# Optimization experiments

Hardware: AMD Instinct MI355X
Metric: run time of the kernel (lower is better)

Reference implementation:

```python
import jax, jax.numpy as jnp
import numpy as np

C = 128
B, H, W = 32, 64, 64


def _lstm(x, Wih, Whh, b, reverse):
    """Batched LSTM, PyTorch gate order (i, f, g, o).
    x: [N, T, C] -> h: [N, T, C]. reverse=True scans backward but returns
    outputs aligned to the original time axis (matches torch bidirectional)."""
    N = x.shape[0]
    Ch = Whh.shape[1]
    xp = jnp.einsum('ntc,gc->ntg', x, Wih) + b  # precomputed input projection [N,T,4C]

    def step(carry, xt):
        h, c = carry
        z = xt + h @ Whh.T
        i, f, g, o = jnp.split(z, 4, axis=-1)
        c = jax.nn.sigmoid(f) * c + jax.nn.sigmoid(i) * jnp.tanh(g)
        h = jax.nn.sigmoid(o) * jnp.tanh(c)
        return (h, c), h

    init = (jnp.zeros((N, Ch), x.dtype), jnp.zeros((N, Ch), x.dtype))
    _, hs = jax.lax.scan(step, init, jnp.swapaxes(xp, 0, 1), reverse=reverse)
    return jnp.swapaxes(hs, 0, 1)


def _conv1x1(x, w, b):
    # x: [B, C, s1, s2]; w: [O, C]; b: [O]
    return jnp.einsum('bcxy,oc->boxy', x, w) + b[None, :, None, None]


def setup_inputs() -> dict:
    key = jax.random.key(0)
    ks = jax.random.split(key, 24)
    k = 1.0 / np.sqrt(C)
    u = lambda kk, shp: jax.random.uniform(kk, shp, jnp.float32, -k, k)
    inp = {'x': jax.random.normal(ks[0], (B, C, H, W), jnp.float32)}
    names = ['vWih_f', 'vWhh_f', 'vb_f', 'vWih_b', 'vWhh_b', 'vb_b',
             'hWih_f', 'hWhh_f', 'hb_f', 'hWih_b', 'hWhh_b', 'hb_b']
    shapes = [(4 * C, C), (4 * C, C), (4 * C,)] * 4
    for i, (n, s) in enumerate(zip(names, shapes)):
        inp[n] = u(ks[1 + i], s)
    for i, n in enumerate(['down', 'up', 'right', 'left']):
        inp['w_' + n] = u(ks[13 + 2 * i], (C, C))
        inp['b_' + n] = u(ks[14 + 2 * i], (C,))
    return inp


def reference(x, vWih_f, vWhh_f, vb_f, vWih_b, vWhh_b, vb_b,
              hWih_f, hWhh_f, hb_f, hWih_b, hWhh_b, hb_b,
              w_down, b_down, w_up, b_up, w_right, b_right, w_left, b_left):
    Bn, Cn, Hn, Wn = x.shape
    xt = jnp.transpose(x, (0, 3, 2, 1))  # [B, W, H, C]  (torch transpose(1,3))

    # vertical LSTM: torch loops i over H, seq over W -> batch rows into B*H
    xv = jnp.transpose(xt, (0, 2, 1, 3)).reshape(Bn * Hn, Wn, Cn)  # [B*H, W, C]
    hv_f = _lstm(xv, vWih_f, vWhh_f, vb_f, False).reshape(Bn, Hn, Wn, Cn)
    hv_b = _lstm(xv, vWih_b, vWhh_b, vb_b, True).reshape(Bn, Hn, Wn, Cn)
    # stack over H at dim2 then transpose(1,3) -> [B, C, H, W]
    x_up = _conv1x1(jnp.transpose(hv_f, (0, 3, 1, 2)), w_up, b_up)
    x_down = _conv1x1(jnp.transpose(hv_b, (0, 3, 1, 2)), w_down, b_down)

    # horizontal LSTM: torch loops i over W, seq over H -> batch cols into B*W
    xh = xt.reshape(Bn * Wn, Hn, Cn)  # [B*W, H, C]
    hh_f = _lstm(xh, hWih_f, hWhh_f, hb_f, False).reshape(Bn, Wn, Hn, Cn)
    hh_b = _lstm(xh, hWih_b, hWhh_b, hb_b, True).reshape(Bn, Wn, Hn, Cn)
    # stack over W at dim2 gives [B, H, W, C]; transpose(1,3) -> [B, C, W, H]
    x_right = _conv1x1(jnp.transpose(hh_f, (0, 3, 1, 2)), w_right, b_right)
    x_left = _conv1x1(jnp.transpose(hh_b, (0, 3, 1, 2)), w_left, b_left)

    return (x_down, x_up, x_right, x_left)
```

## Files before the change

### kernel.cpp

```cpp
#include <hip/hip_runtime.h>
#include <stdint.h>

#define CDIM   128
#define NSEQ   2048
#define TLEN   64
#define PIXTOT (32*64*64)
#define OUTSZ  (32*128*64*64)

typedef short bf16x8 __attribute__((ext_vector_type(8)));
typedef float f32x4  __attribute__((ext_vector_type(4)));

__device__ __forceinline__ uint16_t f2bf(float f) {
  union { float f; uint32_t u; } v; v.f = f;
  uint32_t u = v.u;
  u += 0x7fffu + ((u >> 16) & 1u);
  return (uint16_t)(u >> 16);
}

__device__ __forceinline__ float sigf(float x) {
  return __builtin_amdgcn_rcpf(1.f + __expf(-x));
}
__device__ __forceinline__ float tanh_(float x) {
  float ax = fabsf(x);
  float e  = __expf(-2.f * ax);
  float t  = (1.f - e) * __builtin_amdgcn_rcpf(1.f + e);
  return copysignf(t, x);
}

__global__ void transpose_x(const float* __restrict__ x, uint16_t* __restrict__ xn) {
  const int h = blockIdx.x, b = blockIdx.y;
  __shared__ float tile[128][65];
  const int tid = threadIdx.x;
  #pragma unroll
  for (int it = 0; it < 32; ++it) {
    int idx = it * 256 + tid;
    int c = idx >> 6, w = idx & 63;
    tile[c][w] = x[(((b * 128 + c) * 64 + h) << 6) + w];
  }
  __syncthreads();
  uint32_t* out = (uint32_t*)(xn + ((size_t)(b * 64 + h) * 64) * 128);
  #pragma unroll
  for (int it = 0; it < 16; ++it) {
    int idx = it * 256 + tid;
    int w = idx >> 6, cd = idx & 63;
    uint32_t lo = f2bf(tile[cd * 2][w]);
    uint32_t hi = f2bf(tile[cd * 2 + 1][w]);
    out[w * 64 + cd] = lo | (hi << 16);
  }
}

struct PrepArgs { const float* s[12]; };

__global__ void prep_weights(PrepArgs a, uint16_t* __restrict__ wbuf,
                             uint16_t* __restrict__ wcbuf) {
  int idx = blockIdx.x * 256 + threadIdx.x;
  if (idx < 524288) {
    int m = idx >> 16;
    wbuf[idx] = f2bf(a.s[m][idx & 65535]);
  } else {
    int j = idx - 524288;
    if (j < 65536) {
      int m = j >> 14;
      wcbuf[j] = f2bf(a.s[8 + m][j & 16383]);
    }
  }
}

__global__ __launch_bounds__(512, 2) void lstm_kernel(
    const uint16_t* __restrict__ xn,
    const uint16_t* __restrict__ wbuf,
    const float* __restrict__ bvf, const float* __restrict__ bvb,
    const float* __restrict__ bhf, const float* __restrict__ bhb,
    uint16_t* __restrict__ hbuf)
{
  const int dir  = blockIdx.y;
  const int seq0 = blockIdx.x * 32;
  const int tid  = threadIdx.x;
  const int wv   = tid >> 6;
  const int lane = tid & 63;
  const int l15  = lane & 15;
  const int l4   = lane >> 4;
  const int mycol = wv * 16 + l15;
  const bool rev   = (dir & 1);
  const bool horiz = (dir >= 2);

  const uint16_t* wih = wbuf + (size_t)(2 * dir) * (512 * 128);
  const uint16_t* whh = wih + 512 * 128;
  const float* bias = (dir == 0) ? bvf : (dir == 1) ? bvb : (dir == 2) ? bhf : bhb;
  uint16_t* hout = hbuf + (size_t)dir * ((size_t)NSEQ * TLEN * 128);

  bf16x8 Bih[4][4], Bhh[4][4];
  {
    const int base = mycol * 128 + l4 * 8;
    #pragma unroll
    for (int g = 0; g < 4; ++g)
      #pragma unroll
      for (int kc = 0; kc < 4; ++kc) {
        Bih[g][kc] = *(const bf16x8*)(wih + base + g * (128 * 128) + kc * 32);
        Bhh[g][kc] = *(const bf16x8*)(whh + base + g * (128 * 128) + kc * 32);
      }
  }
  float bia[4];
  #pragma unroll
  for (int g = 0; g < 4; ++g) bia[g] = bias[mycol + 128 * g];

  __shared__ __attribute__((aligned(16))) uint16_t hlds[2][32][136];
  for (int i = tid; i < 2 * 32 * 136; i += 512) ((uint16_t*)hlds)[i] = 0;
  __syncthreads();

  int xbase[2];
  #pragma unroll
  for (int mt = 0; mt < 2; ++mt) {
    int seq = seq0 + mt * 16 + l15;
    xbase[mt] = horiz ? (((seq >> 6) * 4096 + (seq & 63)) * 128)
                      : (seq * (64 * 128));
  }
  const int tstride = horiz ? (64 * 128) : 128;

  float cst[2][4];
  #pragma unroll
  for (int mt = 0; mt < 2; ++mt)
    #pragma unroll
    for (int r = 0; r < 4; ++r) cst[mt][r] = 0.f;

  const f32x4 vzero = {0.f, 0.f, 0.f, 0.f};

  for (int step = 0; step < 64; ++step) {
    const int t = rev ? (63 - step) : step;
    const int cur = step & 1, nxt = cur ^ 1;

    f32x4 acc[2][4];
    #pragma unroll
    for (int mt = 0; mt < 2; ++mt)
      #pragma unroll
      for (int g = 0; g < 4; ++g) acc[mt][g] = vzero;

    #pragma unroll
    for (int kc = 0; kc < 4; ++kc) {
      bf16x8 ax[2], ah[2];
      #pragma unroll
      for (int mt = 0; mt < 2; ++mt) {
        ax[mt] = *(const bf16x8*)(xn + xbase[mt] + t * tstride + kc * 32 + l4 * 8);
        ah[mt] = *(const bf16x8*)(&hlds[cur][mt * 16 + l15][kc * 32 + l4 * 8]);
      }
      #pragma unroll
      for (int mt = 0; mt < 2; ++mt)
        #pragma unroll
        for (int g = 0; g < 4; ++g) {
          acc[mt][g] = __builtin_amdgcn_mfma_f32_16x16x32_bf16(ax[mt], Bih[g][kc], acc[mt][g], 0, 0, 0);
          acc[mt][g] = __builtin_amdgcn_mfma_f32_16x16x32_bf16(ah[mt], Bhh[g][kc], acc[mt][g], 0, 0, 0);
        }
    }

    #pragma unroll
    for (int mt = 0; mt < 2; ++mt)
      #pragma unroll
      for (int r = 0; r < 4; ++r) {
        float zi = acc[mt][0][r] + bia[0];
        float zf = acc[mt][1][r] + bia[1];
        float zg = acc[mt][2][r] + bia[2];
        float zo = acc[mt][3][r] + bia[3];
        float c = sigf(zf) * cst[mt][r] + sigf(zi) * tanh_(zg);
        cst[mt][r] = c;
        float h = sigf(zo) * tanh_(c);
        hlds[nxt][mt * 16 + l4 * 4 + r][mycol] = f2bf(h);
      }
    __syncthreads();

    {
      int sq = tid >> 4, c8 = (tid & 15) * 8;
      bf16x8 v = *(const bf16x8*)(&hlds[nxt][sq][c8]);
      *(bf16x8*)(hout + ((size_t)(seq0 + sq) * 64 + t) * 128 + c8) = v;
    }
  }
}

__global__ __launch_bounds__(256, 2) void conv_kernel(
    const uint16_t* __restrict__ hbuf, const uint16_t* __restrict__ wc,
    const float* __restrict__ b_down, const float* __restrict__ b_up,
    const float* __restrict__ b_right, const float* __restrict__ b_left,
    float* __restrict__ out)
{
  const int d   = blockIdx.y;
  const int P0  = blockIdx.x * 128;
  const int tid = threadIdx.x;
  const int wv = tid >> 6, lane = tid & 63, l15 = lane & 15, l4 = lane >> 4;

  const int lstm_dir = (d == 0) ? 1 : (d == 1) ? 0 : d;
  const uint16_t* hb = hbuf + (size_t)lstm_dir * ((size_t)NSEQ * TLEN * 128);
  const uint16_t* w  = wc + d * (128 * 128);
  const float* bias = (d == 0) ? b_down : (d == 1) ? b_up : (d == 2) ? b_right : b_left;
  float* outp = out + (size_t)d * OUTSZ;

  bf16x8 Bf[2][4];
  float bc[2];
  #pragma unroll
  for (int j = 0; j < 2; ++j) {
    int o = (2 * wv + j) * 16 + l15;
    bc[j] = bias[o];
    #pragma unroll
    for (int kc = 0; kc < 4; ++kc)
      Bf[j][kc] = *(const bf16x8*)(w + o * 128 + kc * 32 + l4 * 8);
  }

  const f32x4 vzero = {0.f, 0.f, 0.f, 0.f};
  f32x4 acc[8][2];
  #pragma unroll
  for (int mt = 0; mt < 8; ++mt) { acc[mt][0] = vzero; acc[mt][1] = vzero; }

  #pragma unroll
  for (int kc = 0; kc < 4; ++kc) {
    bf16x8 A[8];
    #pragma unroll
    for (int mt = 0; mt < 8; ++mt) {
      int p = P0 + mt * 16 + l15;
      A[mt] = *(const bf16x8*)(hb + (size_t)p * 128 + kc * 32 + l4 * 8);
    }
    #pragma unroll
    for (int mt = 0; mt < 8; ++mt)
      #pragma unroll
      for (int j = 0; j < 2; ++j)
        acc[mt][j] = __builtin_amdgcn_mfma_f32_16x16x32_bf16(A[mt], Bf[j][kc], acc[mt][j], 0, 0, 0);
  }

  __shared__ __attribute__((aligned(16))) float olds[128][128];
  #pragma unroll
  for (int mt = 0; mt < 8; ++mt)
    #pragma unroll
    for (int j = 0; j < 2; ++j) {
      int o = (2 * wv + j) * 16 + l15;
      f32x4 v = acc[mt][j] + bc[j];
      int chunk = mt * 4 + l4;
      int phys = chunk ^ (o & 31);
      *(f32x4*)(&olds[o][phys << 2]) = v;
    }
  __syncthreads();

  const int bb = P0 >> 12, s0 = P0 & 4095;
  float* obase = outp + ((size_t)bb * 128) * 4096 + s0;
  #pragma unroll
  for (int it = 0; it < 16; ++it) {
    int flat = (it * 256 + tid) * 4;
    int o = flat >> 7, s = flat & 127;
    int phys = (s >> 2) ^ (o & 31);
    f32x4 v = *(const f32x4*)(&olds[o][phys << 2]);
    *(f32x4*)(obase + (size_t)o * 4096 + s) = v;
  }
}

extern "C" void kernel_launch(void* const* d_in, const int* in_sizes, int n_in,
                              void* d_out, int out_size, void* d_ws, size_t ws_size,
                              hipStream_t stream) {
  const float* x = (const float*)d_in[0];
  uint16_t* ws    = (uint16_t*)d_ws;
  uint16_t* xn    = ws;
  uint16_t* wbuf  = xn + 16777216;
  uint16_t* wcbuf = wbuf + 524288;
  uint16_t* hbuf  = wcbuf + 65536;

  transpose_x<<<dim3(64, 32), 256, 0, stream>>>(x, xn);

  PrepArgs pa;
  const int widx[12] = {1, 2, 4, 5, 7, 8, 10, 11, 13, 15, 17, 19};
  for (int i = 0; i < 12; ++i) pa.s[i] = (const float*)d_in[widx[i]];
  prep_weights<<<2304, 256, 0, stream>>>(pa, wbuf, wcbuf);

  lstm_kernel<<<dim3(64, 4), 512, 0, stream>>>(
      xn, wbuf,
      (const float*)d_in[3], (const float*)d_in[6],
      (const float*)d_in[9], (const float*)d_in[12],
      hbuf);

  conv_kernel<<<dim3(1024, 4), 256, 0, stream>>>(
      hbuf, wcbuf,
      (const float*)d_in[14], (const float*)d_in[16],
      (const float*)d_in[18], (const float*)d_in[20],
      (float*)d_out);
}
```

Measured before the change: 629.0 us.

## Prefetch LSTM inputs, batch hidden-state stores via LDS ring, shrink conv staging

The LSTM loop now loads the next timestep's input fragments one step ahead, using double-buffered registers, so global-load latency overlaps the current step's MFMAs. Hidden states go into an 8-slot XOR-swizzled LDS ring, which avoids bank conflicts and defers the global write of each slot instead of storing right after the barrier. The conv epilogue stages output through a half-size padded LDS tile in two passes, lowering shared-memory use and likely raising occupancy. The cost is more registers and extra barriers in the conv kernel.

```diff
diff --git a/kernel.cpp b/kernel.cpp
--- a/kernel.cpp
+++ b/kernel.cpp
@@ -1,10 +1,6 @@
 #include <hip/hip_runtime.h>
 #include <stdint.h>
 
-#define CDIM   128
-#define NSEQ   2048
-#define TLEN   64
-#define PIXTOT (32*64*64)
 #define OUTSZ  (32*128*64*64)
 
 typedef short bf16x8 __attribute__((ext_vector_type(8)));
@@ -87,7 +83,7 @@
   const uint16_t* wih = wbuf + (size_t)(2 * dir) * (512 * 128);
   const uint16_t* whh = wih + 512 * 128;
   const float* bias = (dir == 0) ? bvf : (dir == 1) ? bvb : (dir == 2) ? bhf : bhb;
-  uint16_t* hout = hbuf + (size_t)dir * ((size_t)NSEQ * TLEN * 128);
+  uint16_t* hout = hbuf + (size_t)dir * ((size_t)2048 * 64 * 128);
 
   bf16x8 Bih[4][4], Bhh[4][4];
   {
@@ -104,8 +100,11 @@
   #pragma unroll
   for (int g = 0; g < 4; ++g) bia[g] = bias[mycol + 128 * g];
 
-  __shared__ __attribute__((aligned(16))) uint16_t hlds[2][32][136];
-  for (int i = tid; i < 2 * 32 * 136; i += 512) ((uint16_t*)hlds)[i] = 0;
+  __shared__ __attribute__((aligned(16))) uint16_t ring[8][32][136];
+  {
+    uint32_t* p = (uint32_t*)&ring[7][0][0];
+    for (int i = tid; i < 2176; i += 512) p[i] = 0;
+  }
   __syncthreads();
 
   int xbase[2];
@@ -123,12 +122,32 @@
     #pragma unroll
     for (int r = 0; r < 4; ++r) cst[mt][r] = 0.f;
 
+  const int drow   = tid >> 4;
+  const int dchunk = tid & 15;
+  const int dpc8   = dchunk ^ ((drow >> 2) & 3);
+
+  auto dump_slot = [&](int g, int s) {
+    bf16x8 v = *(const bf16x8*)(&ring[s][drow][dpc8 * 8]);
+    int stepl = g * 8 + s;
+    int t = rev ? 63 - stepl : stepl;
+    *(bf16x8*)(hout + ((size_t)(seq0 + drow) * 64 + t) * 128 + dchunk * 8) = v;
+  };
+
+  const int swz = (l15 >> 2) & 3;
   const f32x4 vzero = {0.f, 0.f, 0.f, 0.f};
 
-  for (int step = 0; step < 64; ++step) {
-    const int t = rev ? (63 - step) : step;
-    const int cur = step & 1, nxt = cur ^ 1;
-
+  auto do_step = [&](int step, bf16x8 (&axc)[2][4], bf16x8 (&axn)[2][4]) {
+    const int tn_l = (step < 63) ? step + 1 : 63;
+    const int tn   = rev ? 63 - tn_l : tn_l;
+    #pragma unroll
+    for (int mt = 0; mt < 2; ++mt)
+      #pragma unroll
+      for (int kc = 0; kc < 4; ++kc)
+        axn[mt][kc] = *(const bf16x8*)(xn + xbase[mt] + tn * tstride + kc * 32 + l4 * 8);
+
+    if (step >= 7) dump_slot(((step + 1) >> 3) - 1, (step + 1) & 7);
+
+    const int prev = (step + 7) & 7;
     f32x4 acc[2][4];
     #pragma unroll
     for (int mt = 0; mt < 2; ++mt)
@@ -137,21 +156,20 @@
 
     #pragma unroll
     for (int kc = 0; kc < 4; ++kc) {
-      bf16x8 ax[2], ah[2];
-      #pragma unroll
-      for (int mt = 0; mt < 2; ++mt) {
-        ax[mt] = *(const bf16x8*)(xn + xbase[mt] + t * tstride + kc * 32 + l4 * 8);
-        ah[mt] = *(const bf16x8*)(&hlds[cur][mt * 16 + l15][kc * 32 + l4 * 8]);
-      }
+      bf16x8 ah[2];
+      #pragma unroll
+      for (int mt = 0; mt < 2; ++mt)
+        ah[mt] = *(const bf16x8*)(&ring[prev][mt * 16 + l15][((kc * 4 + l4) ^ swz) * 8]);
       #pragma unroll
       for (int mt = 0; mt < 2; ++mt)
         #pragma unroll
         for (int g = 0; g < 4; ++g) {
-          acc[mt][g] = __builtin_amdgcn_mfma_f32_16x16x32_bf16(ax[mt], Bih[g][kc], acc[mt][g], 0, 0, 0);
-          acc[mt][g] = __builtin_amdgcn_mfma_f32_16x16x32_bf16(ah[mt], Bhh[g][kc], acc[mt][g], 0, 0, 0);
+          acc[mt][g] = __builtin_amdgcn_mfma_f32_16x16x32_bf16(axc[mt][kc], Bih[g][kc], acc[mt][g], 0, 0, 0);
+          acc[mt][g] = __builtin_amdgcn_mfma_f32_16x16x32_bf16(ah[mt],      Bhh[g][kc], acc[mt][g], 0, 0, 0);
         }
     }
 
+    const int slot = step & 7;
     #pragma unroll
     for (int mt = 0; mt < 2; ++mt)
       #pragma unroll
@@ -163,16 +181,27 @@
         float c = sigf(zf) * cst[mt][r] + sigf(zi) * tanh_(zg);
         cst[mt][r] = c;
         float h = sigf(zo) * tanh_(c);
-        hlds[nxt][mt * 16 + l4 * 4 + r][mycol] = f2bf(h);
+        int row = mt * 16 + l4 * 4 + r;
+        ring[slot][row][((mycol >> 3) ^ l4) * 8 + (mycol & 7)] = f2bf(h);
       }
     __syncthreads();
-
-    {
-      int sq = tid >> 4, c8 = (tid & 15) * 8;
-      bf16x8 v = *(const bf16x8*)(&hlds[nxt][sq][c8]);
-      *(bf16x8*)(hout + ((size_t)(seq0 + sq) * 64 + t) * 128 + c8) = v;
-    }
-  }
+  };
+
+  bf16x8 axA[2][4], axB[2][4];
+  {
+    const int t0 = rev ? 63 : 0;
+    #pragma unroll
+    for (int mt = 0; mt < 2; ++mt)
+      #pragma unroll
+      for (int kc = 0; kc < 4; ++kc)
+        axA[mt][kc] = *(const bf16x8*)(xn + xbase[mt] + t0 * tstride + kc * 32 + l4 * 8);
+  }
+  for (int s2 = 0; s2 < 64; s2 += 2) {
+    do_step(s2,     axA, axB);
+    do_step(s2 + 1, axB, axA);
+  }
+  #pragma unroll
+  for (int s = 1; s < 8; ++s) dump_slot(7, s);
 }
 
 __global__ __launch_bounds__(256, 2) void conv_kernel(
@@ -187,7 +216,7 @@
   const int wv = tid >> 6, lane = tid & 63, l15 = lane & 15, l4 = lane >> 4;
 
   const int lstm_dir = (d == 0) ? 1 : (d == 1) ? 0 : d;
-  const uint16_t* hb = hbuf + (size_t)lstm_dir * ((size_t)NSEQ * TLEN * 128);
+  const uint16_t* hb = hbuf + (size_t)lstm_dir * ((size_t)2048 * 64 * 128);
   const uint16_t* w  = wc + d * (128 * 128);
   const float* bias = (d == 0) ? b_down : (d == 1) ? b_up : (d == 2) ? b_right : b_left;
   float* outp = out + (size_t)d * OUTSZ;
@@ -223,28 +252,27 @@
         acc[mt][j] = __builtin_amdgcn_mfma_f32_16x16x32_bf16(A[mt], Bf[j][kc], acc[mt][j], 0, 0, 0);
   }
 
-  __shared__ __attribute__((aligned(16))) float olds[128][128];
-  #pragma unroll
-  for (int mt = 0; mt < 8; ++mt)
-    #pragma unroll
-    for (int j = 0; j < 2; ++j) {
-      int o = (2 * wv + j) * 16 + l15;
-      f32x4 v = acc[mt][j] + bc[j];
-      int chunk = mt * 4 + l4;
-      int phys = chunk ^ (o & 31);
-      *(f32x4*)(&olds[o][phys << 2]) = v;
-    }
-  __syncthreads();
-
+  __shared__ __attribute__((aligned(16))) float olds[64][132];
   const int bb = P0 >> 12, s0 = P0 & 4095;
   float* obase = outp + ((size_t)bb * 128) * 4096 + s0;
-  #pragma unroll
-  for (int it = 0; it < 16; ++it) {
-    int flat = (it * 256 + tid) * 4;
-    int o = flat >> 7, s = flat & 127;
-    int phys = (s >> 2) ^ (o & 31);
-    f32x4 v = *(const f32x4*)(&olds[o][phys << 2]);
-    *(f32x4*)(obase + (size_t)o * 4096 + s) = v;
+
+  #pragma unroll
+  for (int j = 0; j < 2; ++j) {
+    if (j) __syncthreads();
+    #pragma unroll
+    for (int mt = 0; mt < 8; ++mt) {
+      f32x4 v = acc[mt][j] + bc[j];
+      *(f32x4*)(&olds[wv * 16 + l15][(mt * 4 + l4) * 4]) = v;
+    }
+    __syncthreads();
+    #pragma unroll
+    for (int it = 0; it < 8; ++it) {
+      int flat = (it * 256 + tid) * 4;
+      int ol = flat >> 7, s = flat & 127;
+      int o = (ol >> 4) * 32 + j * 16 + (ol & 15);
+      f32x4 v = *(const f32x4*)(&olds[ol][s]);
+      *(f32x4*)(obase + (size_t)o * 4096 + s) = v;
+    }
   }
 }
 
```

Measured after the change: 601.3 us. 4.4% less time.
